# Kernel tuning notes

Measured on AMD Instinct MI355X. Metric: run time of the kernel, lower is better.

Reference implementation:

```python
import jax, jax.numpy as jnp
import numpy as np

B, T, N, FI = 2, 16, 256, 1
H, NHEAD, L = 64, 4, 2
MID, LOW, FOUT = 32, 16, 1


def layer_norm(x, g, b, eps=1e-5):
    m = jnp.mean(x, axis=-1, keepdims=True)
    v = jnp.var(x, axis=-1, keepdims=True)
    return (x - m) / jnp.sqrt(v + eps) * g + b


def setup_inputs() -> dict:
    key = jax.random.key(0)
    ks = jax.random.split(key, 24)
    s = 0.05
    inp = {
        'x_seq': jax.random.normal(ks[0], (B, T, N, FI), jnp.float32),
        'edge_index': jax.random.randint(ks[1], (2, 16), 0, N),
        'Wi': jax.random.normal(ks[2], (FI, H), jnp.float32) * s,
        'bi': jnp.zeros((H,), jnp.float32),
        'Wqkv': jax.random.normal(ks[3], (L, H, 3 * H), jnp.float32) * s,
        'bqkv': jnp.zeros((L, 3 * H), jnp.float32),
        'Wo': jax.random.normal(ks[4], (L, H, H), jnp.float32) * s,
        'bo': jnp.zeros((L, H), jnp.float32),
        'ln1_g': jnp.ones((L, H), jnp.float32),
        'ln1_b': jnp.zeros((L, H), jnp.float32),
        'W1': jax.random.normal(ks[5], (L, H, 4 * H), jnp.float32) * s,
        'b1': jnp.zeros((L, 4 * H), jnp.float32),
        'W2': jax.random.normal(ks[6], (L, 4 * H, H), jnp.float32) * s,
        'b2': jnp.zeros((L, H), jnp.float32),
        'ln2_g': jnp.ones((L, H), jnp.float32),
        'ln2_b': jnp.zeros((L, H), jnp.float32),
        'dW1': jax.random.normal(ks[7], (H, MID), jnp.float32) * s,
        'db1': jnp.zeros((MID,), jnp.float32),
        'dW2': jax.random.normal(ks[8], (MID, LOW), jnp.float32) * s,
        'db2': jnp.zeros((LOW,), jnp.float32),
        'dW3': jax.random.normal(ks[9], (LOW, FOUT), jnp.float32) * s,
        'db3': jnp.zeros((FOUT,), jnp.float32),
    }
    return inp


def reference(x_seq, edge_index, Wi, bi, Wqkv, bqkv, Wo, bo, ln1_g, ln1_b,
              W1, b1, W2, b2, ln2_g, ln2_b, dW1, db1, dW2, db2, dW3, db3):
    b, t, n, _ = x_seq.shape
    dh = H // NHEAD
    # input projection
    x = x_seq @ Wi + bi  # [B,T,N,H]
    # sinusoidal time positional encoding (broadcast over nodes)
    pos = jnp.arange(t, dtype=jnp.float32)[:, None]
    div = jnp.exp(jnp.arange(0, H, 2, dtype=jnp.float32) * (-jnp.log(10000.0) / H))
    tp = jnp.zeros((t, H), jnp.float32)
    tp = tp.at[:, 0::2].set(jnp.sin(pos * div)).at[:, 1::2].set(jnp.cos(pos * div))
    x = x + tp[None, :, None, :]
    S = t * n
    x = x.reshape(b, S, H)
    # block-causal additive bias: position i cannot attend to strictly future timesteps
    t_idx = jnp.arange(S) // n
    bias = jnp.where(t_idx[None, :] > t_idx[:, None], -jnp.inf, 0.0).astype(x.dtype)
    inv_sqrt_dh = 1.0 / jnp.sqrt(jnp.asarray(dh, x.dtype))
    for l in range(L):
        qkv = x @ Wqkv[l] + bqkv[l]  # [B,S,3H]
        q, k, v = jnp.split(qkv, 3, axis=-1)
        q = q.reshape(b, S, NHEAD, dh).transpose(0, 2, 1, 3)
        k = k.reshape(b, S, NHEAD, dh).transpose(0, 2, 1, 3)
        v = v.reshape(b, S, NHEAD, dh).transpose(0, 2, 1, 3)
        scores = jnp.einsum('bhqd,bhkd->bhqk', q, k) * inv_sqrt_dh + bias
        attn = jax.nn.softmax(scores, axis=-1)
        o = jnp.einsum('bhqk,bhkd->bhqd', attn, v)
        o = o.transpose(0, 2, 1, 3).reshape(b, S, H)
        o = o @ Wo[l] + bo[l]
        x = layer_norm(x + o, ln1_g[l], ln1_b[l])
        f = jax.nn.relu(x @ W1[l] + b1[l]) @ W2[l] + b2[l]
        x = layer_norm(x + f, ln2_g[l], ln2_b[l])
    last = x.reshape(b, t, n, H)[:, -1]  # [B,N,H]
    h = jax.nn.relu(last @ dW1 + db1)
    h = jax.nn.relu(h @ dW2 + db2)
    return h @ dW3 + db3  # [B,N,1]
```

## Files before the change

kernel.cpp:

```cpp
#include <hip/hip_runtime.h>
#include <math.h>


namespace {
constexpr int T_ = 16, N_ = 256, S_ = 4096;
constexpr int PAIRS = 136;

constexpr size_t OFF_A    = 0;
constexpr size_t OFF_BT   = 192;
constexpr size_t OFF_XB   = 3264;
constexpr size_t OFF_X    = 5632;
constexpr size_t OFF_QKV  = 529920;
constexpr size_t OFF_P0   = 2102784;
constexpr size_t OFF_PM1  = 3675648;
constexpr size_t OFF_PL1  = 3708416;
constexpr size_t OFF_PA1  = 3741184;
constexpr size_t OFF_WT   = 4265472;

typedef float  f32x16 __attribute__((ext_vector_type(16)));
typedef short  short8 __attribute__((ext_vector_type(8)));

__device__ inline float wave_sum(float v) {
#pragma unroll
  for (int off = 32; off > 0; off >>= 1) v += __shfl_xor(v, off, 64);
  return v;
}
__device__ inline unsigned bf16_rne(float f) {
  unsigned u = __float_as_uint(f);
  return (u + 0x7FFFu + ((u >> 16) & 1u)) >> 16;
}
__device__ inline unsigned pack2(float a, float b) {
  return bf16_rne(a) | (bf16_rne(b) << 16);
}
__device__ inline f32x16 zero16() {
  f32x16 z;
#pragma unroll
  for (int i = 0; i < 16; ++i) z[i] = 0.f;
  return z;
}
__device__ inline float pe_val(int t, int h) {
  float div = __expf((float)(h & ~1) * (-0.14391156831212787f));
  float arg = (float)t * div;
  return (h & 1) ? cosf(arg) : sinf(arg);
}
__device__ inline float rebuild(short h, short l) {
  return __uint_as_float(((unsigned)(unsigned short)h) << 16) +
         __uint_as_float(((unsigned)(unsigned short)l) << 16);
}
__device__ __forceinline__ void split4_store(short* hp, short* lp,
                                             float v0, float v1, float v2, float v3) {
  unsigned u0 = __float_as_uint(v0), u1 = __float_as_uint(v1);
  unsigned u2 = __float_as_uint(v2), u3 = __float_as_uint(v3);
  float r0 = v0 - __uint_as_float(u0 & 0xFFFF0000u);
  float r1 = v1 - __uint_as_float(u1 & 0xFFFF0000u);
  float r2 = v2 - __uint_as_float(u2 & 0xFFFF0000u);
  float r3 = v3 - __uint_as_float(u3 & 0xFFFF0000u);
  *(uint2*)hp = make_uint2((u0 >> 16) | (u1 & 0xFFFF0000u),
                           (u2 >> 16) | (u3 & 0xFFFF0000u));
  *(uint2*)lp = make_uint2(pack2(r0, r1), pack2(r2, r3));
}
__device__ __forceinline__ f32x16 gemm_tile(
    const short* __restrict__ Wh, const short* __restrict__ Wl, int tileRow,
    int inDim, int nkt, const short* Bh, const short* Bl, int bstride,
    int l31, int hi) {
  f32x16 C = zero16();
  for (int kt = 0; kt < nkt; ++kt) {
    int ko = kt * 16 + 8 * hi;
    short8 Ah = *(const short8*)&Wh[tileRow * inDim + ko];
    short8 Al = *(const short8*)&Wl[tileRow * inDim + ko];
    short8 Bh8 = *(const short8*)&Bh[l31 * bstride + ko];
    short8 Bl8 = *(const short8*)&Bl[l31 * bstride + ko];
    C = __builtin_amdgcn_mfma_f32_32x32x16_bf16(Ah, Bh8, C, 0, 0, 0);
    C = __builtin_amdgcn_mfma_f32_32x32x16_bf16(Al, Bh8, C, 0, 0, 0);
    C = __builtin_amdgcn_mfma_f32_32x32x16_bf16(Ah, Bl8, C, 0, 0, 0);
  }
  return C;
}

__global__ __launch_bounds__(256, 4) void k_attn0s(
    const float* __restrict__ x_seq, const float* __restrict__ Wi,
    const float* __restrict__ bi, const float* __restrict__ Wqkv,
    const float* __restrict__ bqkv, const float* __restrict__ Wo,
    const float* __restrict__ W1, const float* __restrict__ W2,
    float* __restrict__ A, float* __restrict__ Bt, float* __restrict__ Xb,
    short* __restrict__ WT, float* __restrict__ P0) {
  int blk = blockIdx.x, tid = threadIdx.x;

  if (blk >= 8 * PAIRS) {
    int t = blk - 8 * PAIRS;
    if (t < 16) {
      if (tid < 192) {
        float acc = bqkv[tid];
#pragma unroll 8
        for (int h = 0; h < 64; ++h)
          acc = fmaf(bi[h] + pe_val(t, h), Wqkv[h * 192 + tid], acc);
        Bt[t * 192 + tid] = acc;
      }
      if (tid < 64) Xb[t * 64 + tid] = bi[tid] + pe_val(t, tid);
    } else if (t == 16) {
      if (tid < 192) {
        float acc = 0.f;
#pragma unroll 8
        for (int h = 0; h < 64; ++h) acc = fmaf(Wi[h], Wqkv[h * 192 + tid], acc);
        A[tid] = acc;
      }
    } else {
      int tb2 = t - 17;
      const float* Wq1 = Wqkv + 64 * 192;
#pragma unroll
      for (int e = 0; e < 4; ++e) {
        int gi = tb2 * 1024 + e * 256 + tid;
        float v; int hdst, ldst;
        if (gi < 4096) {
          int o = gi >> 6, i = gi & 63; v = Wo[i * 64 + o];
          hdst = gi; ldst = gi + 4096;
        } else if (gi < 20480) {
          int li = gi - 4096; int o = li >> 6, i = li & 63; v = W1[i * 256 + o];
          hdst = 8192 + li; ldst = 24576 + li;
        } else if (gi < 36864) {
          int li = gi - 20480; int o = li >> 8, i = li & 255; v = W2[i * 64 + o];
          hdst = 40960 + li; ldst = 57344 + li;
        } else {
          int li = gi - 36864; int o = li >> 6, i = li & 63; v = Wq1[i * 192 + o];
          hdst = 73728 + li; ldst = 86016 + li;
        }
        unsigned u = __float_as_uint(v);
        WT[hdst] = (short)(u >> 16);
        WT[ldst] = (short)bf16_rne(v - __uint_as_float(u & 0xFFFF0000u));
      }
    }
    return;
  }

  __shared__ float4 xk4[64];
  __shared__ float peq[64], pek[64];
  __shared__ float red[8];
  __shared__ float scal[6];

  int bh = blk / PAIRS, pair = blk % PAIRS;
  int b = bh >> 2, h = bh & 3;
  int tq = 0, p = pair;
  while (p >= tq + 1) { p -= tq + 1; ++tq; }
  int kt = p;

  if (tid < 64)
    xk4[tid] = *(const float4*)(x_seq + (size_t)(b * S_ + kt * N_) + 4 * tid);
  else if (tid < 128)
    peq[tid - 64] = bi[tid - 64] + pe_val(tq, tid - 64);
  else if (tid < 192)
    pek[tid - 128] = bi[tid - 128] + pe_val(kt, tid - 128);
  __syncthreads();

  {
    float xv = ((const float*)xk4)[tid];
    float mn = xv, mx = xv;
#pragma unroll
    for (int off = 32; off > 0; off >>= 1) {
      mn = fminf(mn, __shfl_xor(mn, off, 64));
      mx = fmaxf(mx, __shfl_xor(mx, off, 64));
    }
    if ((tid & 63) == 0) { red[tid >> 6] = mn; red[4 + (tid >> 6)] = mx; }
  }
  {
    float aq = 0.f, ak = 0.f, bq = 0.f, bk = 0.f;
    if (tid < 16) {
      int cq = h * 16 + tid, ck = 64 + h * 16 + tid;
#pragma unroll 8
      for (int hh = 0; hh < 64; ++hh) {
        float wq = Wqkv[hh * 192 + cq], wk = Wqkv[hh * 192 + ck];
        aq = fmaf(Wi[hh], wq, aq);
        ak = fmaf(Wi[hh], wk, ak);
        bq = fmaf(peq[hh], wq, bq);
        bk = fmaf(pek[hh], wk, bk);
      }
      bq += bqkv[cq]; bk += bqkv[ck];
    }
    float pa = aq * ak, pb = aq * bk, pg = ak * bq, pd = bq * bk;
#pragma unroll
    for (int off = 8; off > 0; off >>= 1) {
      pa += __shfl_xor(pa, off, 64);
      pb += __shfl_xor(pb, off, 64);
      pg += __shfl_xor(pg, off, 64);
      pd += __shfl_xor(pd, off, 64);
    }
    __syncthreads();
    if (tid == 0) {
      const float k2 = 0.36067376022224085f;
      scal[0] = k2 * pa; scal[1] = k2 * pb;
      scal[2] = k2 * pg; scal[3] = k2 * pd;
      scal[4] = fminf(fminf(red[0], red[1]), fminf(red[2], red[3]));
      scal[5] = fmaxf(fmaxf(red[4], red[5]), fmaxf(red[6], red[7]));
    }
  }
  __syncthreads();

  float x = x_seq[b * S_ + tq * N_ + tid];
  float a = fmaf(scal[0], x, scal[2]);
  float xext = (a >= 0.f) ? scal[5] : scal[4];
  float axext = a * xext;
  float Mg = axext + fmaf(scal[1], x, scal[3]);
  float sp0 = 0.f, sp1 = 0.f, sp2 = 0.f, sp3 = 0.f;
  float sx0 = 0.f, sx1 = 0.f, sx2 = 0.f, sx3 = 0.f;
#pragma unroll 8
  for (int j = 0; j < 64; ++j) {
    float4 xv = xk4[j];
    float e0 = __builtin_amdgcn_exp2f(fmaf(a, xv.x, -axext));
    float e1 = __builtin_amdgcn_exp2f(fmaf(a, xv.y, -axext));
    float e2 = __builtin_amdgcn_exp2f(fmaf(a, xv.z, -axext));
    float e3 = __builtin_amdgcn_exp2f(fmaf(a, xv.w, -axext));
    sp0 += e0; sp1 += e1; sp2 += e2; sp3 += e3;
    sx0 = fmaf(xv.x, e0, sx0); sx1 = fmaf(xv.y, e1, sx1);
    sx2 = fmaf(xv.z, e2, sx2); sx3 = fmaf(xv.w, e3, sx3);
  }
  size_t pb2 = ((size_t)(bh * 16 + tq) * 16 + kt) * 768;
  P0[pb2 + tid]       = Mg;
  P0[pb2 + 256 + tid] = (sp0 + sp1) + (sp2 + sp3);
  P0[pb2 + 512 + tid] = (sx0 + sx1) + (sx2 + sx3);
}

__global__ __launch_bounds__(256, 2) void k_fused0(
    const float* __restrict__ P0, const float* __restrict__ A,
    const float* __restrict__ Bt, const float* __restrict__ Xb,
    const float* __restrict__ x_seq, const float* __restrict__ Wi,
    const float* __restrict__ bo, const float* __restrict__ g1,
    const float* __restrict__ be1, const float* __restrict__ bb1,
    const float* __restrict__ bb2, const float* __restrict__ g2,
    const float* __restrict__ be2, const float* __restrict__ bq1,
    const short* __restrict__ WT,
    float* __restrict__ X, float* __restrict__ QKV) {
  __shared__ short qbh[32][72], qbl[32][72];
  __shared__ short xsh[32][72], xsl[32][72];
  __shared__ short hsh[32][264], hsl[32][264];
  __shared__ float ys[16][68];

  const short* WoTh = WT;          const short* WoTl = WT + 4096;
  const short* W1Th = WT + 8192;   const short* W1Tl = WT + 24576;
  const short* W2Th = WT + 40960;  const short* W2Tl = WT + 57344;
  const short* WqTh = WT + 73728;  const short* WqTl = WT + 86016;

  int blk = blockIdx.x;
  int b = blk >> 8, t = (blk >> 4) & 15, n0 = (blk & 15) * 16;
  int gbase = b * S_ + t * N_ + n0;
  int tid = threadIdx.x;
  int w = tid >> 6, lane = tid & 63, l31 = lane & 31, hi = lane >> 5;

  for (int i = tid; i < 16 * 72; i += 256) {
    (&qbh[16][0])[i] = 0; (&qbl[16][0])[i] = 0;
    (&xsh[16][0])[i] = 0; (&xsl[16][0])[i] = 0;
  }
  for (int i = tid; i < 16 * 264; i += 256) {
    (&hsh[16][0])[i] = 0; (&hsl[16][0])[i] = 0;
  }

  {
    int r = tid & 15, hh = (tid >> 4) & 3, d4 = tid >> 6;
    int n = n0 + r, bh4 = b * 4 + hh;
    size_t pbase = ((size_t)(bh4 * 16 + t) * 16) * 768 + n;
    float M = -INFINITY;
    for (int kt = 0; kt <= t; ++kt)
      M = fmaxf(M, P0[pbase + (size_t)kt * 768]);
    float D = 0.f, SX = 0.f, c0 = 0.f, c1 = 0.f, c2 = 0.f, c3 = 0.f;
    for (int kt = 0; kt <= t; ++kt) {
      size_t pb = pbase + (size_t)kt * 768;
      float wgt = __builtin_amdgcn_exp2f(P0[pb] - M);
      float wsp = wgt * P0[pb + 256];
      D += wsp;
      SX = fmaf(wgt, P0[pb + 512], SX);
      float4 bv = *(const float4*)(Bt + kt * 192 + 128 + hh * 16 + d4 * 4);
      c0 = fmaf(wsp, bv.x, c0); c1 = fmaf(wsp, bv.y, c1);
      c2 = fmaf(wsp, bv.z, c2); c3 = fmaf(wsp, bv.w, c3);
    }
    float invD = 1.f / D;
    float4 av = *(const float4*)(A + 128 + hh * 16 + d4 * 4);
    float o0 = fmaf(SX, av.x, c0) * invD;
    float o1 = fmaf(SX, av.y, c1) * invD;
    float o2 = fmaf(SX, av.z, c2) * invD;
    float o3 = fmaf(SX, av.w, c3) * invD;
    split4_store(&qbh[r][hh * 16 + d4 * 4], &qbl[r][hh * 16 + d4 * 4],
                 o0, o1, o2, o3);
  }
  __syncthreads();

  if (w < 2) {
    f32x16 C = gemm_tile(WoTh, WoTl, w * 32 + l31, 64, 4,
                         &qbh[0][0], &qbl[0][0], 72, l31, hi);
    if (l31 < 16) {
#pragma unroll
      for (int g = 0; g < 4; ++g)
        *(float4*)&ys[l31][w * 32 + g * 8 + 4 * hi] =
            make_float4(C[4 * g], C[4 * g + 1], C[4 * g + 2], C[4 * g + 3]);
    }
  }
  __syncthreads();

  {
    int c = tid & 63, grp = tid >> 6;
    float xb_c = Xb[t * 64 + c], wi_c = Wi[c], bo_c = bo[c];
    float g1c = g1[c], be1c = be1[c];
#pragma unroll
    for (int rr = 0; rr < 4; ++rr) {
      int row = grp * 4 + rr;
      float xv = x_seq[gbase + row];
      float val = ys[row][c] + bo_c + fmaf(xv, wi_c, xb_c);
      float mean = wave_sum(val) * (1.f / 64.f);
      float dv = val - mean;
      float var = wave_sum(dv * dv) * (1.f / 64.f);
      float xn = dv * rsqrtf(var + 1e-5f) * g1c + be1c;
      unsigned u = __float_as_uint(xn);
      xsh[row][c] = (short)(u >> 16);
      xsl[row][c] = (short)bf16_rne(xn - __uint_as_float(u & 0xFFFF0000u));
    }
  }
  __syncthreads();

#pragma unroll
  for (int ti = 0; ti < 2; ++ti) {
    int tt = w + 4 * ti;
    f32x16 C = gemm_tile(W1Th, W1Tl, tt * 32 + l31, 64, 4,
                         &xsh[0][0], &xsl[0][0], 72, l31, hi);
    if (l31 < 16) {
#pragma unroll
      for (int g = 0; g < 4; ++g) {
        int cb = tt * 32 + g * 8 + 4 * hi;
        float v0 = fmaxf(C[4 * g + 0] + bb1[cb + 0], 0.f);
        float v1 = fmaxf(C[4 * g + 1] + bb1[cb + 1], 0.f);
        float v2 = fmaxf(C[4 * g + 2] + bb1[cb + 2], 0.f);
        float v3 = fmaxf(C[4 * g + 3] + bb1[cb + 3], 0.f);
        split4_store(&hsh[l31][cb], &hsl[l31][cb], v0, v1, v2, v3);
      }
    }
  }
  __syncthreads();

  if (w < 2) {
    f32x16 C = gemm_tile(W2Th, W2Tl, w * 32 + l31, 256, 16,
                         &hsh[0][0], &hsl[0][0], 264, l31, hi);
    if (l31 < 16) {
#pragma unroll
      for (int g = 0; g < 4; ++g)
        *(float4*)&ys[l31][w * 32 + g * 8 + 4 * hi] =
            make_float4(C[4 * g], C[4 * g + 1], C[4 * g + 2], C[4 * g + 3]);
    }
  }
  __syncthreads();

  {
    int c = tid & 63, grp = tid >> 6;
    float b2c = bb2[c], g2c = g2[c], be2c = be2[c];
#pragma unroll
    for (int rr = 0; rr < 4; ++rr) {
      int row = grp * 4 + rr;
      float val = ys[row][c] + b2c + rebuild(xsh[row][c], xsl[row][c]);
      float mean = wave_sum(val) * (1.f / 64.f);
      float dv = val - mean;
      float var = wave_sum(dv * dv) * (1.f / 64.f);
      float xn = dv * rsqrtf(var + 1e-5f) * g2c + be2c;
      unsigned u = __float_as_uint(xn);
      qbh[row][c] = (short)(u >> 16);
      qbl[row][c] = (short)bf16_rne(xn - __uint_as_float(u & 0xFFFF0000u));
      if (t == 15) X[(size_t)(gbase + row) * 64 + c] = xn;
    }
  }
  __syncthreads();

  {
    int tlA = (t == 15) ? w : (2 + w);
    int ntl = (t == 15 && w < 2) ? 2 : 1;
    for (int ti = 0; ti < ntl; ++ti) {
      int tt = ti ? (w + 4) : tlA;
      f32x16 C = gemm_tile(WqTh, WqTl, tt * 32 + l31, 64, 4,
                           &qbh[0][0], &qbl[0][0], 72, l31, hi);
      if (l31 < 16) {
        size_t rb = (size_t)(gbase + l31) * 192;
#pragma unroll
        for (int g = 0; g < 4; ++g) {
          int cb = tt * 32 + g * 8 + 4 * hi;
          float4 o = make_float4(C[4 * g + 0] + bq1[cb + 0],
                                 C[4 * g + 1] + bq1[cb + 1],
                                 C[4 * g + 2] + bq1[cb + 2],
                                 C[4 * g + 3] + bq1[cb + 3]);
          *(float4*)&QKV[rb + cb] = o;
        }
      }
    }
  }
}

__global__ __launch_bounds__(256, 4) void k_attn1(const float* __restrict__ QKV,
    float* __restrict__ PM, float* __restrict__ PL, float* __restrict__ PACC) {
  __shared__ short KH[2][256][8];
  __shared__ short KL[2][256][8];
  __shared__ short VT[32][264];
  int blk = blockIdx.x;
  int bh = blk >> 4, kt = blk & 15;
  const int tq = 15;
  int b = bh >> 2, h = bh & 3;
  int tid = threadIdx.x, w = tid >> 6, lane = tid & 63;
  int l31 = lane & 31, hi = lane >> 5;
  const size_t qkvbase = (size_t)b * S_ * 192;

  for (int i = tid; i < 16 * 264; i += 256) (&VT[16][0])[i] = 0;
  {
    const float* kp = QKV + qkvbase + (size_t)(kt * N_ + tid) * 192 + 64 + h * 16;
    float kf[16], vf[16];
#pragma unroll
    for (int i = 0; i < 4; ++i) {
      float4 k4 = *(const float4*)(kp + 4 * i);
      kf[4 * i] = k4.x; kf[4 * i + 1] = k4.y; kf[4 * i + 2] = k4.z; kf[4 * i + 3] = k4.w;
      float4 v4 = *(const float4*)(kp + 64 + 4 * i);
      vf[4 * i] = v4.x; vf[4 * i + 1] = v4.y; vf[4 * i + 2] = v4.z; vf[4 * i + 3] = v4.w;
    }
    short8 kh0, kh1, kl0, kl1;
#pragma unroll
    for (int i = 0; i < 8; ++i) {
      unsigned ht0 = __float_as_uint(kf[i]) & 0xFFFF0000u;
      kh0[i] = (short)(ht0 >> 16);
      kl0[i] = (short)bf16_rne(kf[i] - __uint_as_float(ht0));
      unsigned ht1 = __float_as_uint(kf[i + 8]) & 0xFFFF0000u;
      kh1[i] = (short)(ht1 >> 16);
      kl1[i] = (short)bf16_rne(kf[i + 8] - __uint_as_float(ht1));
    }
    *(short8*)&KH[0][tid][0] = kh0;
    *(short8*)&KH[1][tid][0] = kh1;
    *(short8*)&KL[0][tid][0] = kl0;
    *(short8*)&KL[1][tid][0] = kl1;
#pragma unroll
    for (int i = 0; i < 16; ++i) VT[i][tid] = (short)bf16_rne(vf[i]);
  }
  __syncthreads();

  const float cscale = 0.36067376022224085f;
  short8 Qh[2], Ql[2];
#pragma unroll
  for (int qs = 0; qs < 2; ++qs) {
    int qloc = w * 64 + qs * 32 + l31;
    const float* qp = QKV + qkvbase + (size_t)(tq * N_ + qloc) * 192 + h * 16 + 8 * hi;
    float4 a4 = *(const float4*)(qp), b4 = *(const float4*)(qp + 4);
    float qf[8] = {a4.x, a4.y, a4.z, a4.w, b4.x, b4.y, b4.z, b4.w};
#pragma unroll
    for (int i = 0; i < 8; ++i) {
      float q = qf[i] * cscale;
      unsigned ht = __float_as_uint(q) & 0xFFFF0000u;
      Qh[qs][i] = (short)(ht >> 16);
      Ql[qs][i] = (short)bf16_rne(q - __uint_as_float(ht));
    }
  }

  f32x16 O0 = zero16(), O1 = zero16();
  float m[2] = {-INFINITY, -INFINITY}, lsum[2] = {0.f, 0.f};

  for (int ks = 0; ks < 8; ++ks) {
    const short8 Kh = *(const short8*)&KH[hi][ks * 32 + l31][0];
    const short8 Kl = *(const short8*)&KL[hi][ks * 32 + l31][0];
    const short8 Va = *(const short8*)&VT[l31][ks * 32 + 8 * hi];
    const short8 Vb = *(const short8*)&VT[l31][ks * 32 + 8 * hi + 16];

#pragma unroll
    for (int qs = 0; qs < 2; ++qs) {
      f32x16 S = zero16();
      S = __builtin_amdgcn_mfma_f32_32x32x16_bf16(Kh, Qh[qs], S, 0, 0, 0);
      S = __builtin_amdgcn_mfma_f32_32x32x16_bf16(Kl, Qh[qs], S, 0, 0, 0);
      S = __builtin_amdgcn_mfma_f32_32x32x16_bf16(Kh, Ql[qs], S, 0, 0, 0);

      float pm = S[0];
#pragma unroll
      for (int r = 1; r < 16; ++r) pm = fmaxf(pm, S[r]);
      pm = fmaxf(pm, __shfl_xor(pm, 32, 64));
      float mq = m[qs];
      if (__any(pm > mq)) {
        float mn = fmaxf(mq, pm);
        float al = __builtin_amdgcn_exp2f(mq - mn);
        m[qs] = mn; mq = mn;
        lsum[qs] *= al;
        if (qs == 0) {
#pragma unroll
          for (int r = 0; r < 16; ++r) O0[r] *= al;
        } else {
#pragma unroll
          for (int r = 0; r < 16; ++r) O1[r] *= al;
        }
      }
      float pr[16], ps = 0.f;
#pragma unroll
      for (int r = 0; r < 16; ++r) {
        pr[r] = __builtin_amdgcn_exp2f(S[r] - mq);
        ps += pr[r];
      }
      lsum[qs] += ps + __shfl_xor(ps, 32, 64);

      unsigned w01 = pack2(pr[0],  pr[1]);
      unsigned w23 = pack2(pr[2],  pr[3]);
      unsigned w45 = pack2(pr[4],  pr[5]);
      unsigned w67 = pack2(pr[6],  pr[7]);
      unsigned w89 = pack2(pr[8],  pr[9]);
      unsigned wab = pack2(pr[10], pr[11]);
      unsigned wcd = pack2(pr[12], pr[13]);
      unsigned wef = pack2(pr[14], pr[15]);
      unsigned e01 = __shfl_xor(w01, 32, 64), e23 = __shfl_xor(w23, 32, 64);
      unsigned e45 = __shfl_xor(w45, 32, 64), e67 = __shfl_xor(w67, 32, 64);
      unsigned e89 = __shfl_xor(w89, 32, 64), eab = __shfl_xor(wab, 32, 64);
      unsigned ecd = __shfl_xor(wcd, 32, 64), eef = __shfl_xor(wef, 32, 64);
      union { short8 s; unsigned u[4]; } P0u, P1u;
      P0u.u[0] = hi ? e45 : w01;
      P0u.u[1] = hi ? e67 : w23;
      P0u.u[2] = hi ? w45 : e01;
      P0u.u[3] = hi ? w67 : e23;
      P1u.u[0] = hi ? ecd : w89;
      P1u.u[1] = hi ? eef : wab;
      P1u.u[2] = hi ? wcd : e89;
      P1u.u[3] = hi ? wef : eab;

      if (qs == 0) {
        O0 = __builtin_amdgcn_mfma_f32_32x32x16_bf16(Va, P0u.s, O0, 0, 0, 0);
        O0 = __builtin_amdgcn_mfma_f32_32x32x16_bf16(Vb, P1u.s, O0, 0, 0, 0);
      } else {
        O1 = __builtin_amdgcn_mfma_f32_32x32x16_bf16(Va, P0u.s, O1, 0, 0, 0);
        O1 = __builtin_amdgcn_mfma_f32_32x32x16_bf16(Vb, P1u.s, O1, 0, 0, 0);
      }
    }
  }

  int slot = blk;
#pragma unroll
  for (int qs = 0; qs < 2; ++qs) {
    int qloc = w * 64 + qs * 32 + l31;
    if (lane < 32) {
      PM[(size_t)slot * 256 + qloc] = m[qs];
      PL[(size_t)slot * 256 + qloc] = lsum[qs];
    }
    float* pa = PACC + (size_t)slot * 4096 + (size_t)qloc * 16;
    float4 lo4, hi4;
    if (qs == 0) {
      lo4 = make_float4(O0[0], O0[1], O0[2], O0[3]);
      hi4 = make_float4(O0[4], O0[5], O0[6], O0[7]);
    } else {
      lo4 = make_float4(O1[0], O1[1], O1[2], O1[3]);
      hi4 = make_float4(O1[4], O1[5], O1[6], O1[7]);
    }
    *(float4*)(pa + 4 * hi)     = lo4;
    *(float4*)(pa + 8 + 4 * hi) = hi4;
  }
}

__global__ __launch_bounds__(256, 2) void k_fused1(
    const float* __restrict__ PM1, const float* __restrict__ PL1,
    const float* __restrict__ PA1,
    const float* __restrict__ Wo, const float* __restrict__ bo,
    const float* __restrict__ g1, const float* __restrict__ be1,
    const float* __restrict__ W1, const float* __restrict__ bb1,
    const float* __restrict__ W2, const float* __restrict__ bb2,
    const float* __restrict__ g2, const float* __restrict__ be2,
    const float* __restrict__ X,
    const float* __restrict__ dW1, const float* __restrict__ db1,
    const float* __restrict__ dW2, const float* __restrict__ db2,
    const float* __restrict__ dW3, const float* __restrict__ db3,
    float* __restrict__ out) {
  __shared__ float os[4][64], rs[4][64], xs[4][64], x2[4][64], hs[4][256];
  __shared__ float h1s[4][32], h2s[4][16];
  int tid = threadIdx.x;
  int bb = blockIdx.x >> 6;
  int nbase = (blockIdx.x & 63) * 4;
  int row0 = bb * S_ + 15 * N_ + nbase;
  size_t base = (size_t)row0 * 64;

  {
    int d = tid & 15, r = (tid >> 4) & 3, h = tid >> 6;
    int n = nbase + r;
    int sb = (bb * 4 + h) * 16;
    float M = -INFINITY;
#pragma unroll
    for (int s = 0; s < 16; ++s) M = fmaxf(M, PM1[(size_t)(sb + s) * 256 + n]);
    float D = 0.f, od = 0.f;
#pragma unroll
    for (int s = 0; s < 16; ++s) {
      float wgt = __builtin_amdgcn_exp2f(PM1[(size_t)(sb + s) * 256 + n] - M);
      D = fmaf(PL1[(size_t)(sb + s) * 256 + n], wgt, D);
      od = fmaf(PA1[(size_t)(sb + s) * 4096 + (size_t)n * 16 + d], wgt, od);
    }
    os[r][h * 16 + d] = od / D;
    rs[tid >> 6][tid & 63] = X[base + tid];
  }
  __syncthreads();

  int c = tid & 63, grp = tid >> 6;
  {
    float a = bo[c];
#pragma unroll 8
    for (int k = 0; k < 64; ++k) a = fmaf(os[grp][k], Wo[k * 64 + c], a);
    float val = a + rs[grp][c];
    float mean = wave_sum(val) * (1.f / 64.f);
    float dv = val - mean;
    float var = wave_sum(dv * dv) * (1.f / 64.f);
    xs[grp][c] = dv * rsqrtf(var + 1e-5f) * g1[c] + be1[c];
  }
  __syncthreads();

  {
    float am0 = bb1[tid], am1 = am0, am2 = am0, am3 = am0;
    for (int k4 = 0; k4 < 16; ++k4) {
      float w0 = W1[(4 * k4 + 0) * 256 + tid];
      float w1v = W1[(4 * k4 + 1) * 256 + tid];
      float w2v = W1[(4 * k4 + 2) * 256 + tid];
      float w3v = W1[(4 * k4 + 3) * 256 + tid];
      float4 x0 = *(const float4*)&xs[0][4 * k4];
      float4 x1 = *(const float4*)&xs[1][4 * k4];
      float4 x2v = *(const float4*)&xs[2][4 * k4];
      float4 x3 = *(const float4*)&xs[3][4 * k4];
      am0 = fmaf(x0.x, w0, am0); am0 = fmaf(x0.y, w1v, am0);
      am0 = fmaf(x0.z, w2v, am0); am0 = fmaf(x0.w, w3v, am0);
      am1 = fmaf(x1.x, w0, am1); am1 = fmaf(x1.y, w1v, am1);
      am1 = fmaf(x1.z, w2v, am1); am1 = fmaf(x1.w, w3v, am1);
      am2 = fmaf(x2v.x, w0, am2); am2 = fmaf(x2v.y, w1v, am2);
      am2 = fmaf(x2v.z, w2v, am2); am2 = fmaf(x2v.w, w3v, am2);
      am3 = fmaf(x3.x, w0, am3); am3 = fmaf(x3.y, w1v, am3);
      am3 = fmaf(x3.z, w2v, am3); am3 = fmaf(x3.w, w3v, am3);
    }
    hs[0][tid] = fmaxf(am0, 0.f);
    hs[1][tid] = fmaxf(am1, 0.f);
    hs[2][tid] = fmaxf(am2, 0.f);
    hs[3][tid] = fmaxf(am3, 0.f);
  }
  __syncthreads();

  {
    float a = bb2[c];
    for (int k4 = 0; k4 < 64; ++k4) {
      float w0 = W2[(4 * k4 + 0) * 64 + c];
      float w1v = W2[(4 * k4 + 1) * 64 + c];
      float w2v = W2[(4 * k4 + 2) * 64 + c];
      float w3v = W2[(4 * k4 + 3) * 64 + c];
      float4 hv = *(const float4*)&hs[grp][4 * k4];
      a = fmaf(hv.x, w0, a); a = fmaf(hv.y, w1v, a);
      a = fmaf(hv.z, w2v, a); a = fmaf(hv.w, w3v, a);
    }
    float val = a + xs[grp][c];
    float mean = wave_sum(val) * (1.f / 64.f);
    float dv = val - mean;
    float var = wave_sum(dv * dv) * (1.f / 64.f);
    x2[grp][c] = dv * rsqrtf(var + 1e-5f) * g2[c] + be2[c];
  }
  __syncthreads();

  if (tid < 128) {
    int r = tid >> 5, mid = tid & 31;
    float a = db1[mid];
#pragma unroll 8
    for (int k = 0; k < 64; ++k) a = fmaf(x2[r][k], dW1[k * 32 + mid], a);
    h1s[r][mid] = fmaxf(a, 0.f);
  }
  __syncthreads();
  if (tid < 64) {
    int r = tid >> 4, low = tid & 15;
    float a = db2[low];
#pragma unroll
    for (int k = 0; k < 32; ++k) a = fmaf(h1s[r][k], dW2[k * 16 + low], a);
    h2s[r][low] = fmaxf(a, 0.f);
  }
  __syncthreads();
  if (tid < 4) {
    float a = db3[0];
#pragma unroll
    for (int k = 0; k < 16; ++k) a = fmaf(h2s[tid][k], dW3[k], a);
    out[bb * 256 + nbase + tid] = a;
  }
}

}

extern "C" void kernel_launch(void* const* d_in, const int* in_sizes, int n_in,
                              void* d_out, int out_size, void* d_ws, size_t ws_size,
                              hipStream_t stream) {
  const float* x_seq = (const float*)d_in[0];
  const float* Wi   = (const float*)d_in[2];
  const float* bi   = (const float*)d_in[3];
  const float* Wqkv = (const float*)d_in[4];
  const float* bqkv = (const float*)d_in[5];
  const float* Wo   = (const float*)d_in[6];
  const float* bo   = (const float*)d_in[7];
  const float* ln1g = (const float*)d_in[8];
  const float* ln1b = (const float*)d_in[9];
  const float* W1   = (const float*)d_in[10];
  const float* b1   = (const float*)d_in[11];
  const float* W2   = (const float*)d_in[12];
  const float* b2   = (const float*)d_in[13];
  const float* ln2g = (const float*)d_in[14];
  const float* ln2b = (const float*)d_in[15];
  const float* dW1  = (const float*)d_in[16];
  const float* db1  = (const float*)d_in[17];
  const float* dW2  = (const float*)d_in[18];
  const float* db2  = (const float*)d_in[19];
  const float* dW3  = (const float*)d_in[20];
  const float* db3  = (const float*)d_in[21];

  float* ws   = (float*)d_ws;
  float* A    = ws + OFF_A;
  float* Bt   = ws + OFF_BT;
  float* Xb   = ws + OFF_XB;
  float* X    = ws + OFF_X;
  float* QKV  = ws + OFF_QKV;
  float* P0   = ws + OFF_P0;
  float* PM1  = ws + OFF_PM1;
  float* PL1  = ws + OFF_PL1;
  float* PA1  = ws + OFF_PA1;
  short* WT   = (short*)(ws + OFF_WT);

  k_attn0s<<<8 * PAIRS + 65, 256, 0, stream>>>(x_seq, Wi, bi, Wqkv, bqkv,
                                               Wo, W1, W2, A, Bt, Xb, WT, P0);
  k_fused0<<<512, 256, 0, stream>>>(P0, A, Bt, Xb, x_seq, Wi,
                                    bo, ln1g, ln1b, b1, b2, ln2g, ln2b,
                                    bqkv + 192, WT, X, QKV);
  k_attn1<<<128, 256, 0, stream>>>(QKV, PM1, PL1, PA1);
  k_fused1<<<128, 256, 0, stream>>>(PM1, PL1, PA1,
                                    Wo + 4096, bo + 64, ln1g + 64, ln1b + 64,
                                    W1 + 64 * 256, b1 + 256, W2 + 256 * 64, b2 + 64,
                                    ln2g + 64, ln2b + 64, X,
                                    dW1, db1, dW2, db2, dW3, db3, (float*)d_out);
}
```

Measured before the change: 72.23 us.

## Fuse layer-0 rank-1 attention precompute into fused0 kernel, drop attn0s launch

Removes the separate k_attn0s kernel and its P0 partials buffer. Each k_fused0 block now recomputes the per-head rank-1 score coefficients, the key min/max and the softmax sums over all causal key timesteps itself, and converts fp32 weights to split bf16 on the fly inside the GEMM tile loads instead of reading pre-transposed copies. Block-to-timestep order is reversed so the heaviest t=15 blocks launch first. This saves one launch plus the global round trip, but adds redundant per-block work and strided, uncoalesced weight loads with conversion arithmetic in the MFMA loops.

```diff
diff --git a/kernel.cpp b/kernel.cpp
--- a/kernel.cpp
+++ b/kernel.cpp
@@ -4,18 +4,12 @@
 
 namespace {
 constexpr int T_ = 16, N_ = 256, S_ = 4096;
-constexpr int PAIRS = 136;
-
-constexpr size_t OFF_A    = 0;
-constexpr size_t OFF_BT   = 192;
-constexpr size_t OFF_XB   = 3264;
+
 constexpr size_t OFF_X    = 5632;
 constexpr size_t OFF_QKV  = 529920;
-constexpr size_t OFF_P0   = 2102784;
 constexpr size_t OFF_PM1  = 3675648;
 constexpr size_t OFF_PL1  = 3708416;
 constexpr size_t OFF_PA1  = 3741184;
-constexpr size_t OFF_WT   = 4265472;
 
 typedef float  f32x16 __attribute__((ext_vector_type(16)));
 typedef short  short8 __attribute__((ext_vector_type(8)));
@@ -59,15 +53,21 @@
                            (u2 >> 16) | (u3 & 0xFFFF0000u));
   *(uint2*)lp = make_uint2(pack2(r0, r1), pack2(r2, r3));
 }
-__device__ __forceinline__ f32x16 gemm_tile(
-    const short* __restrict__ Wh, const short* __restrict__ Wl, int tileRow,
-    int inDim, int nkt, const short* Bh, const short* Bl, int bstride,
-    int l31, int hi) {
+__device__ __forceinline__ f32x16 gemm_tile_g(
+    const float* __restrict__ W, int outDim, int tileBase, int nkt,
+    const short* Bh, const short* Bl, int bstride, int l31, int hi) {
   f32x16 C = zero16();
+  int colr = tileBase + l31;
   for (int kt = 0; kt < nkt; ++kt) {
     int ko = kt * 16 + 8 * hi;
-    short8 Ah = *(const short8*)&Wh[tileRow * inDim + ko];
-    short8 Al = *(const short8*)&Wl[tileRow * inDim + ko];
+    short8 Ah, Al;
+#pragma unroll
+    for (int e = 0; e < 8; ++e) {
+      float v = W[(ko + e) * outDim + colr];
+      unsigned u = __float_as_uint(v);
+      Ah[e] = (short)(u >> 16);
+      Al[e] = (short)bf16_rne(v - __uint_as_float(u & 0xFFFF0000u));
+    }
     short8 Bh8 = *(const short8*)&Bh[l31 * bstride + ko];
     short8 Bl8 = *(const short8*)&Bl[l31 * bstride + ko];
     C = __builtin_amdgcn_mfma_f32_32x32x16_bf16(Ah, Bh8, C, 0, 0, 0);
@@ -77,225 +77,190 @@
   return C;
 }
 
-__global__ __launch_bounds__(256, 4) void k_attn0s(
+__global__ __launch_bounds__(256, 2) void k_fused0(
     const float* __restrict__ x_seq, const float* __restrict__ Wi,
     const float* __restrict__ bi, const float* __restrict__ Wqkv,
-    const float* __restrict__ bqkv, const float* __restrict__ Wo,
-    const float* __restrict__ W1, const float* __restrict__ W2,
-    float* __restrict__ A, float* __restrict__ Bt, float* __restrict__ Xb,
-    short* __restrict__ WT, float* __restrict__ P0) {
+    const float* __restrict__ bqkv,
+    const float* __restrict__ Wo, const float* __restrict__ bo,
+    const float* __restrict__ g1, const float* __restrict__ be1,
+    const float* __restrict__ W1, const float* __restrict__ bb1,
+    const float* __restrict__ W2, const float* __restrict__ bb2,
+    const float* __restrict__ g2, const float* __restrict__ be2,
+    float* __restrict__ X, float* __restrict__ QKV) {
+  __shared__ __align__(16) char smem[56576];
+  short (*qbh)[72]  = (short(*)[72])(smem + 0);
+  short (*qbl)[72]  = (short(*)[72])(smem + 4608);
+  short (*xsh)[72]  = (short(*)[72])(smem + 9216);
+  short (*xsl)[72]  = (short(*)[72])(smem + 13824);
+  short (*hsh)[264] = (short(*)[264])(smem + 18432);
+  short (*hsl)[264] = (short(*)[264])(smem + 35328);
+  float (*ys)[68]   = (float(*)[68])(smem + 52224);
+  float (*keys)[256] = (float(*)[256])(smem + 18432);
+  float (*pek)[64]   = (float(*)[64])(smem + 52224);
+  float (*Btv)[64]   = (float(*)[64])(smem + 35328);
+  float (*Bkk)[64]   = (float(*)[64])(smem + 39424);
+  float* xbv    = (float*)(smem + 43520);
+  float* AqS    = (float*)(smem + 43776);
+  float* AkS    = (float*)(smem + 44032);
+  float* AvS    = (float*)(smem + 44288);
+  float* BqS    = (float*)(smem + 44544);
+  float* alphaS = (float*)(smem + 44800);
+  float* gamS   = (float*)(smem + 44816);
+  float* betaS  = (float*)(smem + 44832);
+  float* deltS  = (float*)(smem + 45088);
+  float* mnS    = (float*)(smem + 45344);
+  float* mxS    = (float*)(smem + 45408);
+
+  const float K2 = 0.36067376022224085f;
+  const float* Wq1 = Wqkv + 64 * 192;
+  const float* bq1 = bqkv + 192;
+
   int blk = blockIdx.x, tid = threadIdx.x;
-
-  if (blk >= 8 * PAIRS) {
-    int t = blk - 8 * PAIRS;
-    if (t < 16) {
-      if (tid < 192) {
-        float acc = bqkv[tid];
-#pragma unroll 8
-        for (int h = 0; h < 64; ++h)
-          acc = fmaf(bi[h] + pe_val(t, h), Wqkv[h * 192 + tid], acc);
-        Bt[t * 192 + tid] = acc;
-      }
-      if (tid < 64) Xb[t * 64 + tid] = bi[tid] + pe_val(t, tid);
-    } else if (t == 16) {
-      if (tid < 192) {
-        float acc = 0.f;
-#pragma unroll 8
-        for (int h = 0; h < 64; ++h) acc = fmaf(Wi[h], Wqkv[h * 192 + tid], acc);
-        A[tid] = acc;
-      }
-    } else {
-      int tb2 = t - 17;
-      const float* Wq1 = Wqkv + 64 * 192;
-#pragma unroll
-      for (int e = 0; e < 4; ++e) {
-        int gi = tb2 * 1024 + e * 256 + tid;
-        float v; int hdst, ldst;
-        if (gi < 4096) {
-          int o = gi >> 6, i = gi & 63; v = Wo[i * 64 + o];
-          hdst = gi; ldst = gi + 4096;
-        } else if (gi < 20480) {
-          int li = gi - 4096; int o = li >> 6, i = li & 63; v = W1[i * 256 + o];
-          hdst = 8192 + li; ldst = 24576 + li;
-        } else if (gi < 36864) {
-          int li = gi - 20480; int o = li >> 8, i = li & 255; v = W2[i * 64 + o];
-          hdst = 40960 + li; ldst = 57344 + li;
-        } else {
-          int li = gi - 36864; int o = li >> 6, i = li & 63; v = Wq1[i * 192 + o];
-          hdst = 73728 + li; ldst = 86016 + li;
-        }
-        unsigned u = __float_as_uint(v);
-        WT[hdst] = (short)(u >> 16);
-        WT[ldst] = (short)bf16_rne(v - __uint_as_float(u & 0xFFFF0000u));
-      }
-    }
-    return;
-  }
-
-  __shared__ float4 xk4[64];
-  __shared__ float peq[64], pek[64];
-  __shared__ float red[8];
-  __shared__ float scal[6];
-
-  int bh = blk / PAIRS, pair = blk % PAIRS;
-  int b = bh >> 2, h = bh & 3;
-  int tq = 0, p = pair;
-  while (p >= tq + 1) { p -= tq + 1; ++tq; }
-  int kt = p;
-
-  if (tid < 64)
-    xk4[tid] = *(const float4*)(x_seq + (size_t)(b * S_ + kt * N_) + 4 * tid);
-  else if (tid < 128)
-    peq[tid - 64] = bi[tid - 64] + pe_val(tq, tid - 64);
-  else if (tid < 192)
-    pek[tid - 128] = bi[tid - 128] + pe_val(kt, tid - 128);
-  __syncthreads();
-
-  {
-    float xv = ((const float*)xk4)[tid];
-    float mn = xv, mx = xv;
-#pragma unroll
-    for (int off = 32; off > 0; off >>= 1) {
-      mn = fminf(mn, __shfl_xor(mn, off, 64));
-      mx = fmaxf(mx, __shfl_xor(mx, off, 64));
-    }
-    if ((tid & 63) == 0) { red[tid >> 6] = mn; red[4 + (tid >> 6)] = mx; }
-  }
-  {
-    float aq = 0.f, ak = 0.f, bq = 0.f, bk = 0.f;
-    if (tid < 16) {
-      int cq = h * 16 + tid, ck = 64 + h * 16 + tid;
-#pragma unroll 8
-      for (int hh = 0; hh < 64; ++hh) {
-        float wq = Wqkv[hh * 192 + cq], wk = Wqkv[hh * 192 + ck];
-        aq = fmaf(Wi[hh], wq, aq);
-        ak = fmaf(Wi[hh], wk, ak);
-        bq = fmaf(peq[hh], wq, bq);
-        bk = fmaf(pek[hh], wk, bk);
-      }
-      bq += bqkv[cq]; bk += bqkv[ck];
-    }
-    float pa = aq * ak, pb = aq * bk, pg = ak * bq, pd = bq * bk;
-#pragma unroll
-    for (int off = 8; off > 0; off >>= 1) {
-      pa += __shfl_xor(pa, off, 64);
-      pb += __shfl_xor(pb, off, 64);
-      pg += __shfl_xor(pg, off, 64);
-      pd += __shfl_xor(pd, off, 64);
-    }
-    __syncthreads();
-    if (tid == 0) {
-      const float k2 = 0.36067376022224085f;
-      scal[0] = k2 * pa; scal[1] = k2 * pb;
-      scal[2] = k2 * pg; scal[3] = k2 * pd;
-      scal[4] = fminf(fminf(red[0], red[1]), fminf(red[2], red[3]));
-      scal[5] = fmaxf(fmaxf(red[4], red[5]), fmaxf(red[6], red[7]));
-    }
-  }
-  __syncthreads();
-
-  float x = x_seq[b * S_ + tq * N_ + tid];
-  float a = fmaf(scal[0], x, scal[2]);
-  float xext = (a >= 0.f) ? scal[5] : scal[4];
-  float axext = a * xext;
-  float Mg = axext + fmaf(scal[1], x, scal[3]);
-  float sp0 = 0.f, sp1 = 0.f, sp2 = 0.f, sp3 = 0.f;
-  float sx0 = 0.f, sx1 = 0.f, sx2 = 0.f, sx3 = 0.f;
-#pragma unroll 8
-  for (int j = 0; j < 64; ++j) {
-    float4 xv = xk4[j];
-    float e0 = __builtin_amdgcn_exp2f(fmaf(a, xv.x, -axext));
-    float e1 = __builtin_amdgcn_exp2f(fmaf(a, xv.y, -axext));
-    float e2 = __builtin_amdgcn_exp2f(fmaf(a, xv.z, -axext));
-    float e3 = __builtin_amdgcn_exp2f(fmaf(a, xv.w, -axext));
-    sp0 += e0; sp1 += e1; sp2 += e2; sp3 += e3;
-    sx0 = fmaf(xv.x, e0, sx0); sx1 = fmaf(xv.y, e1, sx1);
-    sx2 = fmaf(xv.z, e2, sx2); sx3 = fmaf(xv.w, e3, sx3);
-  }
-  size_t pb2 = ((size_t)(bh * 16 + tq) * 16 + kt) * 768;
-  P0[pb2 + tid]       = Mg;
-  P0[pb2 + 256 + tid] = (sp0 + sp1) + (sp2 + sp3);
-  P0[pb2 + 512 + tid] = (sx0 + sx1) + (sx2 + sx3);
-}
-
-__global__ __launch_bounds__(256, 2) void k_fused0(
-    const float* __restrict__ P0, const float* __restrict__ A,
-    const float* __restrict__ Bt, const float* __restrict__ Xb,
-    const float* __restrict__ x_seq, const float* __restrict__ Wi,
-    const float* __restrict__ bo, const float* __restrict__ g1,
-    const float* __restrict__ be1, const float* __restrict__ bb1,
-    const float* __restrict__ bb2, const float* __restrict__ g2,
-    const float* __restrict__ be2, const float* __restrict__ bq1,
-    const short* __restrict__ WT,
-    float* __restrict__ X, float* __restrict__ QKV) {
-  __shared__ short qbh[32][72], qbl[32][72];
-  __shared__ short xsh[32][72], xsl[32][72];
-  __shared__ short hsh[32][264], hsl[32][264];
-  __shared__ float ys[16][68];
-
-  const short* WoTh = WT;          const short* WoTl = WT + 4096;
-  const short* W1Th = WT + 8192;   const short* W1Tl = WT + 24576;
-  const short* W2Th = WT + 40960;  const short* W2Tl = WT + 57344;
-  const short* WqTh = WT + 73728;  const short* WqTl = WT + 86016;
-
-  int blk = blockIdx.x;
-  int b = blk >> 8, t = (blk >> 4) & 15, n0 = (blk & 15) * 16;
+  int b = blk >> 8, t = 15 - ((blk >> 4) & 15), n0 = (blk & 15) * 16;
   int gbase = b * S_ + t * N_ + n0;
-  int tid = threadIdx.x;
   int w = tid >> 6, lane = tid & 63, l31 = lane & 31, hi = lane >> 5;
 
   for (int i = tid; i < 16 * 72; i += 256) {
     (&qbh[16][0])[i] = 0; (&qbl[16][0])[i] = 0;
     (&xsh[16][0])[i] = 0; (&xsl[16][0])[i] = 0;
   }
-  for (int i = tid; i < 16 * 264; i += 256) {
-    (&hsh[16][0])[i] = 0; (&hsl[16][0])[i] = 0;
-  }
-
-  {
-    int r = tid & 15, hh = (tid >> 4) & 3, d4 = tid >> 6;
-    int n = n0 + r, bh4 = b * 4 + hh;
-    size_t pbase = ((size_t)(bh4 * 16 + t) * 16) * 768 + n;
-    float M = -INFINITY;
-    for (int kt = 0; kt <= t; ++kt)
-      M = fmaxf(M, P0[pbase + (size_t)kt * 768]);
+#pragma unroll
+  for (int i = 0; i < 4; ++i) {
+    int u = tid + 256 * i;
+    pek[u >> 6][u & 63] = pe_val(u >> 6, u & 63);
+  }
+  __syncthreads();
+
+  for (int c = tid; c < 192; c += 256) {
+    float acc = 0.f;
+#pragma unroll 8
+    for (int hh = 0; hh < 64; ++hh) acc = fmaf(Wi[hh], Wqkv[hh * 192 + c], acc);
+    if (c < 64) AqS[c] = acc;
+    else if (c < 128) AkS[c - 64] = acc;
+    else AvS[c - 128] = acc;
+  }
+  if (tid < 64) {
+    float acc = bqkv[tid];
+#pragma unroll 8
+    for (int hh = 0; hh < 64; ++hh)
+      acc = fmaf(bi[hh] + pek[t][hh], Wqkv[hh * 192 + tid], acc);
+    BqS[tid] = acc;
+    xbv[tid] = bi[tid] + pek[t][tid];
+  }
+  for (int u = tid; u < (t + 1) * 128; u += 256) {
+    int kt = u >> 7, cc = u & 127, col = 64 + cc;
+    float acc = bqkv[col];
+#pragma unroll 8
+    for (int hh = 0; hh < 64; ++hh)
+      acc = fmaf(bi[hh] + pek[kt][hh], Wqkv[hh * 192 + col], acc);
+    if (cc < 64) Bkk[kt][cc] = acc; else Btv[kt][cc - 64] = acc;
+  }
+  for (int u = tid; u < (t + 1) * 256; u += 256)
+    keys[u >> 8][u & 255] = x_seq[(size_t)b * S_ + u];
+  __syncthreads();
+
+  if (tid < 4) {
+    float al = 0.f, gm = 0.f;
+#pragma unroll
+    for (int i = 0; i < 16; ++i) {
+      al = fmaf(AqS[tid * 16 + i], AkS[tid * 16 + i], al);
+      gm = fmaf(AkS[tid * 16 + i], BqS[tid * 16 + i], gm);
+    }
+    alphaS[tid] = K2 * al; gamS[tid] = K2 * gm;
+  }
+  if (tid < 64 && (tid & 15) <= t) {
+    int h = tid >> 4, kt = tid & 15;
+    float be = 0.f, de = 0.f;
+#pragma unroll
+    for (int i = 0; i < 16; ++i) {
+      float bk = Bkk[kt][h * 16 + i];
+      be = fmaf(AqS[h * 16 + i], bk, be);
+      de = fmaf(BqS[h * 16 + i], bk, de);
+    }
+    betaS[h * 16 + kt] = K2 * be; deltS[h * 16 + kt] = K2 * de;
+  }
+  {
+    int kt = tid >> 4, s16 = tid & 15;
+    if (kt <= t) {
+      float mn = 1e30f, mx = -1e30f;
+#pragma unroll
+      for (int j = 0; j < 16; ++j) {
+        float v = keys[kt][s16 * 16 + j];
+        mn = fminf(mn, v); mx = fmaxf(mx, v);
+      }
+#pragma unroll
+      for (int off = 1; off < 16; off <<= 1) {
+        mn = fminf(mn, __shfl_xor(mn, off, 64));
+        mx = fmaxf(mx, __shfl_xor(mx, off, 64));
+      }
+      if (s16 == 0) { mnS[kt] = mn; mxS[kt] = mx; }
+    }
+  }
+  __syncthreads();
+
+  {
+    int h = w, q = lane >> 2, s = lane & 3;
+    float x = keys[t][n0 + q];
+    float a = fmaf(alphaS[h], x, gamS[h]);
+    float M = -1e30f;
+    for (int kt = 0; kt <= t; ++kt) {
+      float xe = (a >= 0.f) ? mxS[kt] : mnS[kt];
+      float Mg = fmaf(a, xe, fmaf(betaS[h * 16 + kt], x, deltS[h * 16 + kt]));
+      M = fmaxf(M, Mg);
+    }
     float D = 0.f, SX = 0.f, c0 = 0.f, c1 = 0.f, c2 = 0.f, c3 = 0.f;
+    int dbase = h * 16 + s * 4;
     for (int kt = 0; kt <= t; ++kt) {
-      size_t pb = pbase + (size_t)kt * 768;
-      float wgt = __builtin_amdgcn_exp2f(P0[pb] - M);
-      float wsp = wgt * P0[pb + 256];
-      D += wsp;
-      SX = fmaf(wgt, P0[pb + 512], SX);
-      float4 bv = *(const float4*)(Bt + kt * 192 + 128 + hh * 16 + d4 * 4);
-      c0 = fmaf(wsp, bv.x, c0); c1 = fmaf(wsp, bv.y, c1);
-      c2 = fmaf(wsp, bv.z, c2); c3 = fmaf(wsp, bv.w, c3);
-    }
+      float off = fmaf(betaS[h * 16 + kt], x, deltS[h * 16 + kt]) - M;
+      const float* kr = &keys[kt][s * 64];
+      float spa = 0.f, spb = 0.f;
+#pragma unroll 8
+      for (int jj = 0; jj < 64; jj += 2) {
+        int j0 = (jj + s * 8) & 63, j1 = (jj + 1 + s * 8) & 63;
+        float x0 = kr[j0], x1 = kr[j1];
+        float p0 = __builtin_amdgcn_exp2f(fmaf(a, x0, off));
+        float p1 = __builtin_amdgcn_exp2f(fmaf(a, x1, off));
+        spa += p0; spb += p1;
+        SX = fmaf(p0, x0, SX); SX = fmaf(p1, x1, SX);
+      }
+      float sp = spa + spb;
+      sp += __shfl_xor(sp, 1, 64);
+      sp += __shfl_xor(sp, 2, 64);
+      D += sp;
+      c0 = fmaf(sp, Btv[kt][dbase + 0], c0);
+      c1 = fmaf(sp, Btv[kt][dbase + 1], c1);
+      c2 = fmaf(sp, Btv[kt][dbase + 2], c2);
+      c3 = fmaf(sp, Btv[kt][dbase + 3], c3);
+    }
+    SX += __shfl_xor(SX, 1, 64);
+    SX += __shfl_xor(SX, 2, 64);
     float invD = 1.f / D;
-    float4 av = *(const float4*)(A + 128 + hh * 16 + d4 * 4);
-    float o0 = fmaf(SX, av.x, c0) * invD;
-    float o1 = fmaf(SX, av.y, c1) * invD;
-    float o2 = fmaf(SX, av.z, c2) * invD;
-    float o3 = fmaf(SX, av.w, c3) * invD;
-    split4_store(&qbh[r][hh * 16 + d4 * 4], &qbl[r][hh * 16 + d4 * 4],
-                 o0, o1, o2, o3);
+    float o0 = fmaf(SX, AvS[dbase + 0], c0) * invD;
+    float o1 = fmaf(SX, AvS[dbase + 1], c1) * invD;
+    float o2 = fmaf(SX, AvS[dbase + 2], c2) * invD;
+    float o3 = fmaf(SX, AvS[dbase + 3], c3) * invD;
+    split4_store(&qbh[q][dbase], &qbl[q][dbase], o0, o1, o2, o3);
   }
   __syncthreads();
 
   if (w < 2) {
-    f32x16 C = gemm_tile(WoTh, WoTl, w * 32 + l31, 64, 4,
-                         &qbh[0][0], &qbl[0][0], 72, l31, hi);
+    f32x16 C = gemm_tile_g(Wo, 64, w * 32, 4, &qbh[0][0], &qbl[0][0], 72, l31, hi);
     if (l31 < 16) {
 #pragma unroll
       for (int g = 0; g < 4; ++g)
         *(float4*)&ys[l31][w * 32 + g * 8 + 4 * hi] =
             make_float4(C[4 * g], C[4 * g + 1], C[4 * g + 2], C[4 * g + 3]);
     }
+  } else {
+    for (int i = tid - 128; i < 16 * 264; i += 128) {
+      (&hsh[16][0])[i] = 0; (&hsl[16][0])[i] = 0;
+    }
   }
   __syncthreads();
 
   {
     int c = tid & 63, grp = tid >> 6;
-    float xb_c = Xb[t * 64 + c], wi_c = Wi[c], bo_c = bo[c];
+    float xb_c = xbv[c], wi_c = Wi[c], bo_c = bo[c];
     float g1c = g1[c], be1c = be1[c];
 #pragma unroll
     for (int rr = 0; rr < 4; ++rr) {
@@ -316,8 +281,7 @@
 #pragma unroll
   for (int ti = 0; ti < 2; ++ti) {
     int tt = w + 4 * ti;
-    f32x16 C = gemm_tile(W1Th, W1Tl, tt * 32 + l31, 64, 4,
-                         &xsh[0][0], &xsl[0][0], 72, l31, hi);
+    f32x16 C = gemm_tile_g(W1, 256, tt * 32, 4, &xsh[0][0], &xsl[0][0], 72, l31, hi);
     if (l31 < 16) {
 #pragma unroll
       for (int g = 0; g < 4; ++g) {
@@ -333,8 +297,7 @@
   __syncthreads();
 
   if (w < 2) {
-    f32x16 C = gemm_tile(W2Th, W2Tl, w * 32 + l31, 256, 16,
-                         &hsh[0][0], &hsl[0][0], 264, l31, hi);
+    f32x16 C = gemm_tile_g(W2, 64, w * 32, 16, &hsh[0][0], &hsl[0][0], 264, l31, hi);
     if (l31 < 16) {
 #pragma unroll
       for (int g = 0; g < 4; ++g)
@@ -368,8 +331,7 @@
     int ntl = (t == 15 && w < 2) ? 2 : 1;
     for (int ti = 0; ti < ntl; ++ti) {
       int tt = ti ? (w + 4) : tlA;
-      f32x16 C = gemm_tile(WqTh, WqTl, tt * 32 + l31, 64, 4,
-                           &qbh[0][0], &qbl[0][0], 72, l31, hi);
+      f32x16 C = gemm_tile_g(Wq1, 192, tt * 32, 4, &qbh[0][0], &qbl[0][0], 72, l31, hi);
       if (l31 < 16) {
         size_t rb = (size_t)(gbase + l31) * 192;
 #pragma unroll
@@ -693,22 +655,15 @@
   const float* db3  = (const float*)d_in[21];
 
   float* ws   = (float*)d_ws;
-  float* A    = ws + OFF_A;
-  float* Bt   = ws + OFF_BT;
-  float* Xb   = ws + OFF_XB;
   float* X    = ws + OFF_X;
   float* QKV  = ws + OFF_QKV;
-  float* P0   = ws + OFF_P0;
   float* PM1  = ws + OFF_PM1;
   float* PL1  = ws + OFF_PL1;
   float* PA1  = ws + OFF_PA1;
-  short* WT   = (short*)(ws + OFF_WT);
-
-  k_attn0s<<<8 * PAIRS + 65, 256, 0, stream>>>(x_seq, Wi, bi, Wqkv, bqkv,
-                                               Wo, W1, W2, A, Bt, Xb, WT, P0);
-  k_fused0<<<512, 256, 0, stream>>>(P0, A, Bt, Xb, x_seq, Wi,
-                                    bo, ln1g, ln1b, b1, b2, ln2g, ln2b,
-                                    bqkv + 192, WT, X, QKV);
+
+  k_fused0<<<512, 256, 0, stream>>>(x_seq, Wi, bi, Wqkv, bqkv,
+                                    Wo, bo, ln1g, ln1b, W1, b1, W2, b2,
+                                    ln2g, ln2b, X, QKV);
   k_attn1<<<128, 256, 0, stream>>>(QKV, PM1, PL1, PA1);
   k_fused1<<<128, 256, 0, stream>>>(PM1, PL1, PA1,
                                     Wo + 4096, bo + 64, ln1g + 64, ln1b + 64,
```

New measurement: 90.96 us. 1.26x slower.
